# Kernel optimization log

Hardware: AMD Instinct MI355X
Metric: run time of the kernel (lower is better)

The kernel has to match this reference:

```python
import jax, jax.numpy as jnp
import numpy as np
from jax import lax

A = 20          # alphabet size (input_size)
L = 512         # max_seq_length
CH = 8          # conv channels
N_LAYERS = 9    # log2(512) conv+pool stages


def setup_inputs() -> dict:
    key = jax.random.key(0)
    ks = jax.random.split(key, 6)
    B = 1024
    idx = jax.random.randint(ks[0], (B, L), 0, A)
    lens = jax.random.randint(ks[1], (B,), L // 4, L + 1)
    masks = jnp.arange(L)[None, :] < lens[:, None]            # [B, L] bool
    # one-hot sequences, zeroed at padded positions (so nonzero() skips them)
    x = jax.nn.one_hot(idx, A, dtype=jnp.float32) * masks[..., None].astype(jnp.float32)
    blosum = jax.random.normal(ks[2], (A, A), jnp.float32)
    blosum = (blosum + blosum.T) * 0.5                        # symmetric like BLOSUM
    lpm = blosum                                              # trainable copy
    pm = jnp.clip(blosum, 0.0)                                # clamp(min=0) constant
    std = jnp.ones((1,), jnp.float32)                         # Gaussian std for row decay
    w0 = jax.random.normal(ks[3], (CH, 1, 3), jnp.float32) * 0.3
    ws = jax.random.normal(ks[4], (N_LAYERS - 1, CH, CH, 3), jnp.float32) * 0.2
    return {"x": x, "masks": masks, "lpm": lpm, "pm": pm, "std": std, "w0": w0, "ws": ws}


def _shift_pos(m, k):
    # target index clamp(s + k, max=L-1): shift right by k, boundary index L-1
    # collects any source in the last k+1 positions (set semantics -> OR).
    head = jnp.zeros(m.shape[:-1] + (k,), dtype=bool)
    body = m[..., : L - k - 1]                                # targets k .. L-2
    last = jnp.any(m[..., L - 1 - k:], axis=-1, keepdims=True)
    return jnp.concatenate([head, body, last], axis=-1)


def _shift_neg(m, k):
    # target index clamp(s - k, min=0)
    first = jnp.any(m[..., : k + 1], axis=-1, keepdims=True)
    body = m[..., k + 1:]                                     # targets 1 .. L-1-k
    tail = jnp.zeros(m.shape[:-1] + (k,), dtype=bool)
    return jnp.concatenate([first, body, tail], axis=-1)


def _column(nz, lpm, pm):
    # Banded substitution scatter: each one-hot row i writes V[i, r] into row r
    # at the same (batch, seq) position. Original nested index_put loops collapse
    # to a single 20x20 matrix V applied via einsum (one-hot => no collisions).
    ii = jnp.arange(A)[:, None]
    rr = jnp.arange(A)[None, :]
    M = jnp.clip(lpm, 0.001, 1.0) * pm
    # up-writes: j in 1..18-i => i < r <= 18 ; down-writes: j in 1..i => r < i
    V = jnp.where((rr > ii) & (rr <= A - 2), M, 0.0) + jnp.where(rr < ii, M.T, 0.0)
    return jnp.einsum('bis,ir->brs', nz, V)


def _row(m, std):
    # Gaussian positional decay: writes exp(-k^2/(2 std^2)) at seq offsets +-k,
    # k = 1,2,3 in order (later k overwrites earlier at clamp collisions).
    row = jnp.zeros(m.shape, jnp.float32)
    for k in (1, 2, 3):
        mk = _shift_pos(m, k) | _shift_neg(m, k)
        vk = jnp.exp(-(k * k) / (2.0 * std * std))[0]
        row = jnp.where(mk, vk, row)
    return row


def _conv1d(h, w):
    # Conv1d(kernel=3, stride=1, pad=1, no bias)
    return lax.conv_general_dilated(h, w, (1,), [(1, 1)],
                                    dimension_numbers=('NCH', 'OIH', 'NCH'))


def _avgpool2(h):
    N, C, Lh = h.shape
    return h.reshape(N, C, Lh // 2, 2).mean(-1)


def reference(x, masks, lpm, pm, std, w0, ws):
    B = x.shape[0]
    xp = jnp.transpose(x, (0, 2, 1))          # [B, 20, L]
    m = xp != 0
    nz = m.astype(xp.dtype)
    h = xp + _column(nz, lpm, pm) + _row(m, std)
    h = h.reshape(B * A, 1, L)
    h = _avgpool2(_conv1d(h, w0))
    for i in range(N_LAYERS - 1):
        h = _avgpool2(_conv1d(h, ws[i]))
    return h.squeeze(-1).reshape(B, A, -1)    # [B, 20, 8]
```

## Files before the change

### kernel.cpp

```cpp
#include <hip/hip_runtime.h>
#include <math.h>

#define LSEQ 512
#define NA 20
#define NCH 8
#define NBLK_IMP 129

__global__ __launch_bounds__(256) void wf_vt_kernel(
    const float* __restrict__ w0,
    const float* __restrict__ wsg,
    const float* __restrict__ lpm,
    const float* __restrict__ pm,
    float* __restrict__ wf,
    float* __restrict__ vtn)
{
    if (blockIdx.x == NBLK_IMP) {
        for (int o = threadIdx.x; o < NA * NA; o += 256) {
            int j = o / NA, a = o % NA;
            float v = 0.f;
            if (a > j && a <= NA - 2)
                v += fminf(fmaxf(lpm[j * NA + a], 0.001f), 1.0f) * pm[j * NA + a];
            if (a < j)
                v += fminf(fmaxf(lpm[a * NA + j], 0.001f), 1.0f) * pm[a * NA + j];
            vtn[o] = v;
        }
        return;
    }

    const int w = threadIdx.x >> 6;
    const int t = threadIdx.x & 63;
    const int s = blockIdx.x * 4 + w;

    __shared__ float s_h[4][LSEQ];
    __shared__ float s_a[4][NCH * 256];
    __shared__ float s_b[4][NCH * 128];
    float* hh = s_h[w];
    float* aa = s_a[w];
    float* bb = s_b[w];

    for (int i = t; i < LSEQ; i += 64) hh[i] = (i == s) ? 1.f : 0.f;
    __syncthreads();

    const int c = t >> 3;
    const int pb = t & 7;

    {
        float q0 = w0[c * 3 + 0], q1 = w0[c * 3 + 1], q2 = w0[c * 3 + 2];
        float wa = q0, wb = q0 + q1, wc2 = q1 + q2, wd = q2;
        for (int p = pb; p < 256; p += 8) {
            int xx = 2 * p;
            float x0 = (xx > 0) ? hh[xx - 1] : 0.f;
            float x1 = hh[xx];
            float x2 = hh[xx + 1];
            float x3 = (xx + 2 < LSEQ) ? hh[xx + 2] : 0.f;
            aa[c * 256 + p] = 0.5f * (wa * x0 + wb * x1 + wc2 * x2 + wd * x3);
        }
    }
    __syncthreads();

    int Lin = 256;
    for (int li = 0; li < 8; ++li) {
        const float* fin = (li & 1) ? bb : aa;
        float* fout = (li & 1) ? aa : bb;
        const int Lout = Lin >> 1;

        float wa[8], wb[8], wc2[8], wd[8];
        const float* wl = wsg + li * 192 + c * 24;
#pragma unroll
        for (int ci = 0; ci < 8; ++ci) {
            float q0 = wl[ci * 3 + 0], q1 = wl[ci * 3 + 1], q2 = wl[ci * 3 + 2];
            wa[ci] = q0; wb[ci] = q0 + q1; wc2[ci] = q1 + q2; wd[ci] = q2;
        }

        for (int p = pb; p < Lout; p += 8) {
            int xx = 2 * p;
            float acc = 0.f;
#pragma unroll
            for (int ci = 0; ci < 8; ++ci) {
                const float* ip = fin + ci * Lin + xx;
                float x0 = (xx > 0) ? ip[-1] : 0.f;
                float x1 = ip[0];
                float x2 = ip[1];
                float x3 = (xx + 2 < Lin) ? ip[2] : 0.f;
                acc += wa[ci] * x0 + wb[ci] * x1 + wc2[ci] * x2 + wd[ci] * x3;
            }
            fout[c * Lout + p] = 0.5f * acc;
        }
        __syncthreads();
        Lin = Lout;
    }

    if (t < NCH && s < LSEQ) wf[t * 512 + s] = aa[t];
}

__global__ __launch_bounds__(256) void main_kernel(
    const float* __restrict__ x,
    const float* __restrict__ vtn,
    const float* __restrict__ g_std,
    const float* __restrict__ wf,
    float* __restrict__ out)
{
    const int b = blockIdx.x;
    const int t = threadIdx.x;
    const int c = t & 7;
    const int seg = t >> 3;
    const int w = t >> 6;
    const int lane = t & 63;

    __shared__ __align__(16) float s_h[NA * 512];
    __shared__ __align__(16) float s_vtn[NA * NA];
    __shared__ float s_part[4 * NA * NCH];
    __shared__ unsigned char s_idx[LSEQ];

    float4 wr[4];
#pragma unroll
    for (int k = 0; k < 4; ++k)
        wr[k] = *(const float4*)(wf + c * 512 + seg * 4 + 128 * k);

    if (t < NA * NA / 4) ((float4*)s_vtn)[t] = ((const float4*)vtn)[t];

    const float4* xb = (const float4*)(x + (size_t)b * LSEQ * NA);
#pragma unroll
    for (int rep = 0; rep < 2; ++rep) {
        int s = t + rep * 256;
        int id = 255;
#pragma unroll
        for (int q = 0; q < 5; ++q) {
            float4 v = xb[s * 5 + q];
            if (v.x > .5f) id = 4 * q + 0;
            if (v.y > .5f) id = 4 * q + 1;
            if (v.z > .5f) id = 4 * q + 2;
            if (v.w > .5f) id = 4 * q + 3;
        }
        s_idx[s] = (unsigned char)id;
    }
    __syncthreads();

    const float stdv = g_std[0];
    const float inv2s2 = 1.f / (2.f * stdv * stdv);
    const float vks[3] = {__expf(-1.f * inv2s2), __expf(-4.f * inv2s2), __expf(-9.f * inv2s2)};

    for (int s = t; s < LSEQ; s += 256) {
        const int ai = s_idx[s];
        const bool valid = ai < NA;
#pragma unroll
        for (int a = 0; a < NA; ++a) {
            float v = valid ? (s_vtn[ai * NA + a] + (a == ai ? 1.f : 0.f)) : 0.f;
            s_h[a * 512 + s] = v;
        }
#pragma unroll
        for (int k = 1; k <= 3; ++k) {
            const float add = vks[k - 1];
            if (s == LSEQ - 1) {
                for (int u = LSEQ - 1 - k; u <= LSEQ - 1; ++u) {
                    int tg = s_idx[u];
                    if (tg < NA)
                        s_h[tg * 512 + s] =
                            (valid ? s_vtn[ai * NA + tg] + (tg == ai ? 1.f : 0.f) : 0.f) + add;
                }
            } else if (s >= k) {
                int tg = s_idx[s - k];
                if (tg < NA)
                    s_h[tg * 512 + s] =
                        (valid ? s_vtn[ai * NA + tg] + (tg == ai ? 1.f : 0.f) : 0.f) + add;
            }
            if (s == 0) {
                for (int u = 0; u <= k; ++u) {
                    int tg = s_idx[u];
                    if (tg < NA)
                        s_h[tg * 512 + s] =
                            (valid ? s_vtn[ai * NA + tg] + (tg == ai ? 1.f : 0.f) : 0.f) + add;
                }
            } else if (s + k < LSEQ) {
                int tg = s_idx[s + k];
                if (tg < NA)
                    s_h[tg * 512 + s] =
                        (valid ? s_vtn[ai * NA + tg] + (tg == ai ? 1.f : 0.f) : 0.f) + add;
            }
        }
    }
    __syncthreads();

#pragma unroll 1
    for (int a = 0; a < NA; ++a) {
        const float* hb = s_h + a * 512 + seg * 4;
        float acc = 0.f;
#pragma unroll
        for (int k = 0; k < 4; ++k) {
            float4 hv = *(const float4*)(hb + 128 * k);
            acc += hv.x * wr[k].x + hv.y * wr[k].y + hv.z * wr[k].z + hv.w * wr[k].w;
        }
        acc += __shfl_xor(acc, 8);
        acc += __shfl_xor(acc, 16);
        acc += __shfl_xor(acc, 32);
        if ((lane >> 3) == 0) s_part[w * (NA * NCH) + a * NCH + c] = acc;
    }
    __syncthreads();

    if (t < NA * NCH)
        out[(size_t)b * (NA * NCH) + t] =
            s_part[t] + s_part[160 + t] + s_part[320 + t] + s_part[480 + t];
}

extern "C" void kernel_launch(void* const* d_in, const int* in_sizes, int n_in,
                              void* d_out, int out_size, void* d_ws, size_t ws_size,
                              hipStream_t stream) {
    const float* x    = (const float*)d_in[0];
    const float* lpm  = (const float*)d_in[2];
    const float* pm   = (const float*)d_in[3];
    const float* stdp = (const float*)d_in[4];
    const float* w0   = (const float*)d_in[5];
    const float* wsg  = (const float*)d_in[6];
    float* out = (float*)d_out;

    const int B = in_sizes[0] / (LSEQ * NA);

    float* vtn = (float*)d_ws;
    float* wfb = (float*)d_ws + 1024;

    wf_vt_kernel<<<dim3(NBLK_IMP + 1), dim3(256), 0, stream>>>(w0, wsg, lpm, pm, wfb, vtn);
    main_kernel<<<dim3(B), dim3(256), 0, stream>>>(x, vtn, stdp, wfb, out);
}
```

Before: 124.7 us.

## Compute effective filter via adjoint backpropagation per output channel

The old code built the composite linear filter (512 taps per output channel) with a forward pass of a one-hot impulse for every sequence position, which took 129 blocks doing full conv/pool chains. The new code runs the transposed (adjoint) conv+pool chain backward from each of the 8 output channels, so only 8 blocks plus the substitution-matrix block are needed. This cuts the preprocessing kernel's work and launch size. The cost is a serial chain of 8 upsampling stages inside a single block, each with low parallelism in its early stages.

```diff
diff --git a/kernel.cpp b/kernel.cpp
--- a/kernel.cpp
+++ b/kernel.cpp
@@ -4,7 +4,6 @@
 #define LSEQ 512
 #define NA 20
 #define NCH 8
-#define NBLK_IMP 129
 
 __global__ __launch_bounds__(256) void wf_vt_kernel(
     const float* __restrict__ w0,
@@ -14,8 +13,10 @@
     float* __restrict__ wf,
     float* __restrict__ vtn)
 {
-    if (blockIdx.x == NBLK_IMP) {
-        for (int o = threadIdx.x; o < NA * NA; o += 256) {
+    const int t = threadIdx.x;
+
+    if (blockIdx.x == NCH) {
+        for (int o = t; o < NA * NA; o += 256) {
             int j = o / NA, a = o % NA;
             float v = 0.f;
             if (a > j && a <= NA - 2)
@@ -27,70 +28,60 @@
         return;
     }
 
-    const int w = threadIdx.x >> 6;
-    const int t = threadIdx.x & 63;
-    const int s = blockIdx.x * 4 + w;
-
-    __shared__ float s_h[4][LSEQ];
-    __shared__ float s_a[4][NCH * 256];
-    __shared__ float s_b[4][NCH * 128];
-    float* hh = s_h[w];
-    float* aa = s_a[w];
-    float* bb = s_b[w];
-
-    for (int i = t; i < LSEQ; i += 64) hh[i] = (i == s) ? 1.f : 0.f;
-    __syncthreads();
-
-    const int c = t >> 3;
-    const int pb = t & 7;
+    const int r = blockIdx.x;
+
+    __shared__ float gA[NCH * 256];
+    __shared__ float gB[NCH * 256];
+    __shared__ float4 s_e[NCH * NCH];
+
+    if (t < NCH) gA[t * 256] = (t == r) ? 1.f : 0.f;
+    __syncthreads();
+
+    int P = 1;
+    for (int step = 0; step < 8; ++step) {
+        const int li = 7 - step;
+        if (t < 64) {
+            const int co = t >> 3, ci = t & 7;
+            const float* wp = wsg + li * 192 + co * 24 + ci * 3;
+            const float a0 = wp[0], a1 = wp[1], a2 = wp[2];
+            s_e[co * 8 + ci] = make_float4(a0 + a1, a2, a1 + a2, a0);
+        }
+        __syncthreads();
+        const float* gi = (step & 1) ? gB : gA;
+        float* go = (step & 1) ? gA : gB;
+        for (int it = t; it < NCH * P; it += 256) {
+            const int ci = it >> step;
+            const int p = it & (P - 1);
+            float accE = 0.f, accO = 0.f;
+#pragma unroll
+            for (int co = 0; co < NCH; ++co) {
+                const float g0 = gi[co * 256 + p];
+                const float gm = (p > 0) ? gi[co * 256 + p - 1] : 0.f;
+                const float gp = (p + 1 < P) ? gi[co * 256 + p + 1] : 0.f;
+                const float4 e = s_e[co * 8 + ci];
+                accE += e.x * g0 + e.y * gm;
+                accO += e.z * g0 + e.w * gp;
+            }
+            *(float2*)(go + ci * 256 + 2 * p) = make_float2(0.5f * accE, 0.5f * accO);
+        }
+        __syncthreads();
+        P <<= 1;
+    }
 
     {
-        float q0 = w0[c * 3 + 0], q1 = w0[c * 3 + 1], q2 = w0[c * 3 + 2];
-        float wa = q0, wb = q0 + q1, wc2 = q1 + q2, wd = q2;
-        for (int p = pb; p < 256; p += 8) {
-            int xx = 2 * p;
-            float x0 = (xx > 0) ? hh[xx - 1] : 0.f;
-            float x1 = hh[xx];
-            float x2 = hh[xx + 1];
-            float x3 = (xx + 2 < LSEQ) ? hh[xx + 2] : 0.f;
-            aa[c * 256 + p] = 0.5f * (wa * x0 + wb * x1 + wc2 * x2 + wd * x3);
-        }
-    }
-    __syncthreads();
-
-    int Lin = 256;
-    for (int li = 0; li < 8; ++li) {
-        const float* fin = (li & 1) ? bb : aa;
-        float* fout = (li & 1) ? aa : bb;
-        const int Lout = Lin >> 1;
-
-        float wa[8], wb[8], wc2[8], wd[8];
-        const float* wl = wsg + li * 192 + c * 24;
-#pragma unroll
-        for (int ci = 0; ci < 8; ++ci) {
-            float q0 = wl[ci * 3 + 0], q1 = wl[ci * 3 + 1], q2 = wl[ci * 3 + 2];
-            wa[ci] = q0; wb[ci] = q0 + q1; wc2[ci] = q1 + q2; wd[ci] = q2;
-        }
-
-        for (int p = pb; p < Lout; p += 8) {
-            int xx = 2 * p;
-            float acc = 0.f;
-#pragma unroll
-            for (int ci = 0; ci < 8; ++ci) {
-                const float* ip = fin + ci * Lin + xx;
-                float x0 = (xx > 0) ? ip[-1] : 0.f;
-                float x1 = ip[0];
-                float x2 = ip[1];
-                float x3 = (xx + 2 < Lin) ? ip[2] : 0.f;
-                acc += wa[ci] * x0 + wb[ci] * x1 + wc2[ci] * x2 + wd[ci] * x3;
-            }
-            fout[c * Lout + p] = 0.5f * acc;
-        }
-        __syncthreads();
-        Lin = Lout;
-    }
-
-    if (t < NCH && s < LSEQ) wf[t * 512 + s] = aa[t];
+        const int p = t;
+        float accE = 0.f, accO = 0.f;
+#pragma unroll
+        for (int co = 0; co < NCH; ++co) {
+            const float g0 = gA[co * 256 + p];
+            const float gm = (p > 0) ? gA[co * 256 + p - 1] : 0.f;
+            const float gp = (p < 255) ? gA[co * 256 + p + 1] : 0.f;
+            const float q0 = w0[co * 3 + 0], q1 = w0[co * 3 + 1], q2 = w0[co * 3 + 2];
+            accE += (q0 + q1) * g0 + q2 * gm;
+            accO += (q1 + q2) * g0 + q0 * gp;
+        }
+        *(float2*)(wf + r * 512 + 2 * p) = make_float2(0.5f * accE, 0.5f * accO);
+    }
 }
 
 __global__ __launch_bounds__(256) void main_kernel(
@@ -218,6 +209,6 @@
     float* vtn = (float*)d_ws;
     float* wfb = (float*)d_ws + 1024;
 
-    wf_vt_kernel<<<dim3(NBLK_IMP + 1), dim3(256), 0, stream>>>(w0, wsg, lpm, pm, wfb, vtn);
+    wf_vt_kernel<<<dim3(NCH + 1), dim3(256), 0, stream>>>(w0, wsg, lpm, pm, wfb, vtn);
     main_kernel<<<dim3(B), dim3(256), 0, stream>>>(x, vtn, stdp, wfb, out);
 }
```

Result: faster. 112.7 us (-9.6%).
